# Optimization experiments

Measured on AMD Instinct MI355X. Metric: run time of the kernel, lower is better.

Reference implementation:

```python
import jax, jax.numpy as jnp
import numpy as np


def _approx_match(xyz1, xyz2):
    """Faithful port of approxmatch_cpu/cuda (auction-style soft bipartite matching).

    xyz1: [b, n, 3], xyz2: [b, m, 3] -> (match [b, n, m], sq_dists [b, n, m])
    """
    b, n, _ = xyz1.shape
    m = xyz2.shape[1]
    factorl = max(n, m) // n  # integer division, as in the CUDA source
    factorr = max(n, m) // m

    # all-pairs squared distances  [b, n, m]
    d2 = jnp.sum((xyz1[:, :, None, :] - xyz2[:, None, :, :]) ** 2, axis=-1)

    # annealing schedule: j = 8 .. -1 -> level = -4^j ; j = -2 -> level = 0
    levels = jnp.asarray([-(4.0 ** j) for j in range(8, -2, -1)] + [0.0],
                         dtype=xyz1.dtype)

    satl0 = jnp.full((b, n), float(factorl), dtype=xyz1.dtype)  # row capacities
    satr0 = jnp.full((b, m), float(factorr), dtype=xyz1.dtype)  # col capacities
    match0 = jnp.zeros((b, n, m), dtype=xyz1.dtype)

    def step(carry, level):
        satl, satr, match = carry
        # weight = exp(level * d2) * saturatedr
        w = jnp.exp(level * d2) * satr[:, None, :]                       # [b,n,m]
        # row-normalize, scale by remaining row capacity
        w = w / (jnp.sum(w, axis=2, keepdims=True) + 1e-9) * satl[:, :, None]
        # column rescale by remaining column capacity
        ss = jnp.sum(w, axis=1) + 1e-9                                   # [b,m]
        w = w * (satr / ss)[:, None, :]
        # deplete capacities
        satl = jnp.maximum(satl - jnp.sum(w, axis=2), 0.0)
        satr = jnp.maximum(satr - jnp.sum(w, axis=1), 0.0)
        return (satl, satr, match + w), None

    (_, _, match), _ = jax.lax.scan(step, (satl0, satr0, match0), levels)
    return match, d2


def setup_inputs() -> dict:
    key = jax.random.key(0)
    k1, k2 = jax.random.split(key)
    b, n, m = 4, 4096, 4096
    return {
        "input1": jax.random.normal(k1, (b, n, 3), dtype=jnp.float32),
        "input2": jax.random.normal(k2, (b, m, 3), dtype=jnp.float32),
        "eps": 0,    # accepted but unused by the original Function
        "iters": 50, # accepted but unused by the original Function
    }


def reference(input1, input2, eps, iters):
    # eps / iters are ignored, matching EarthMoverDistanceFunction.apply(xyz1, xyz2)
    match, d2 = _approx_match(input1, input2)
    dist = jnp.sqrt(jnp.maximum(d2, 1e-12))  # matchcost uses euclidean (sqrt) distance
    return jnp.sum(match * dist, axis=(1, 2))  # cost per batch element, [b]
```

## Files before the change

### kernel.cpp

```cpp
#include <hip/hip_runtime.h>

#define BLOCK 256
#define IC    64
#define RPT   4
#define ROWS  (BLOCK*RPT)
#define RBLK  64

__device__ __forceinline__ float wave_reduce_add(float v) {
#pragma unroll
    for (int off = 32; off > 0; off >>= 1) v += __shfl_down(v, off, 64);
    return v;
}
__device__ __forceinline__ float lg2(float x) { return __builtin_amdgcn_logf(x); }
__device__ __forceinline__ float ex2(float x) { return __builtin_amdgcn_exp2f(x); }

__device__ __forceinline__ void load_rows(const float* p, float* x, float* y, float* z) {
    float4 v0 = *(const float4*)p;
    float4 v1 = *(const float4*)(p + 4);
    float4 v2 = *(const float4*)(p + 8);
    x[0]=v0.x; x[1]=v0.w; x[2]=v1.z; x[3]=v2.y;
    y[0]=v0.y; y[1]=v1.x; y[2]=v1.w; y[3]=v2.z;
    z[0]=v0.z; z[1]=v1.y; z[2]=v2.x; z[3]=v2.w;
}

__global__ __launch_bounds__(BLOCK)
void emd_init(float* __restrict__ satl, float* __restrict__ satr,
              float* __restrict__ out, float fl, float fr,
              int b, int n, int m) {
    int idx = blockIdx.x * blockDim.x + threadIdx.x;
    if (idx < b * n) satl[idx] = fl;
    if (idx < b * m) satr[idx] = fr;
    if (idx < b)     out[idx]  = 0.f;
}


__global__ __launch_bounds__(BLOCK, 4)
void emd_pass2(const float* __restrict__ xyzO, const float* __restrict__ xyzS,
               const float* __restrict__ lgw, float* __restrict__ Pout,
               float ls, float wconst, float thr, int nO, int nS, int bnO)
{
    __shared__ float4 sh[IC];
    const int bb = blockIdx.z, chunk = blockIdx.y;

    const int j0 = blockIdx.x * ROWS + threadIdx.x * RPT;
    float x[RPT], y[RPT], z[RPT], acc[RPT];
    load_rows(xyzO + ((size_t)bb * nO + j0) * 3, x, y, z);

    const float* xs = xyzS + (size_t)bb * nS * 3;
    for (int t = threadIdx.x; t < IC; t += BLOCK) {
        int i = chunk * IC + t;
        float w = lgw ? lgw[(size_t)bb * nS + i] : wconst;
        sh[t] = make_float4(xs[3*i], xs[3*i+1], xs[3*i+2], w);
    }
    __syncthreads();

#pragma unroll
    for (int r = 0; r < RPT; ++r) acc[r] = 0.f;
#pragma unroll 2
    for (int tb = 0; tb < IC; tb += 4) {
        float4 q0 = sh[tb+0], q1 = sh[tb+1], q2 = sh[tb+2], q3 = sh[tb+3];
        float d0[RPT], d1[RPT], d2v[RPT], d3[RPT];
        float dmin = 1e30f;
#pragma unroll
        for (int r = 0; r < RPT; ++r) {
            float dx, dy, dz;
            dx=x[r]-q0.x; dy=y[r]-q0.y; dz=z[r]-q0.z; d0[r]=fmaf(dz,dz,fmaf(dy,dy,dx*dx));
            dx=x[r]-q1.x; dy=y[r]-q1.y; dz=z[r]-q1.z; d1[r]=fmaf(dz,dz,fmaf(dy,dy,dx*dx));
            dx=x[r]-q2.x; dy=y[r]-q2.y; dz=z[r]-q2.z; d2v[r]=fmaf(dz,dz,fmaf(dy,dy,dx*dx));
            dx=x[r]-q3.x; dy=y[r]-q3.y; dz=z[r]-q3.z; d3[r]=fmaf(dz,dz,fmaf(dy,dy,dx*dx));
            dmin = fminf(dmin, fminf(fminf(d0[r], d1[r]), fminf(d2v[r], d3[r])));
        }
        if (__any(dmin < thr)) {
#pragma unroll
            for (int r = 0; r < RPT; ++r) {
                acc[r] += ex2(fmaf(d0[r],  ls, q0.w));
                acc[r] += ex2(fmaf(d1[r],  ls, q1.w));
                acc[r] += ex2(fmaf(d2v[r], ls, q2.w));
                acc[r] += ex2(fmaf(d3[r],  ls, q3.w));
            }
        }
    }
    *(float4*)&Pout[(size_t)chunk * bnO + (size_t)bb * nO + j0] =
        make_float4(acc[0], acc[1], acc[2], acc[3]);
}

__global__ __launch_bounds__(BLOCK, 4)
void emd_fused(const float* __restrict__ xyz1, const float* __restrict__ xyz2,
               const float* __restrict__ lgr2, const float* __restrict__ lgsn,
               float* __restrict__ P3a, float* __restrict__ P3b,
               float* __restrict__ P1p,
               float lsA, float lsB, float thr, int n, int m, int bn)
{
    __shared__ float4 sh[IC];
    __shared__ float  shB[IC];
    const int bb = blockIdx.z, chunk = blockIdx.y;

    const int i0 = blockIdx.x * ROWS + threadIdx.x * RPT;
    float x[RPT], y[RPT], z[RPT];
    load_rows(xyz1 + ((size_t)bb * n + i0) * 3, x, y, z);

    const float* x2 = xyz2 + (size_t)bb * m * 3;
    for (int t = threadIdx.x; t < IC; t += BLOCK) {
        int j = chunk * IC + t;
        size_t rj = (size_t)bb * m + j;
        sh[t]  = make_float4(x2[3*j], x2[3*j+1], x2[3*j+2], lgr2[rj]);
        shB[t] = lgsn[rj];
    }
    __syncthreads();

    float s1[RPT], s2[RPT], r1[RPT];
#pragma unroll
    for (int r = 0; r < RPT; ++r) { s1[r] = 0.f; s2[r] = 0.f; r1[r] = 0.f; }
#pragma unroll 2
    for (int tb = 0; tb < IC; tb += 4) {
        float4 q0 = sh[tb+0], q1 = sh[tb+1], q2 = sh[tb+2], q3 = sh[tb+3];
        float lb0 = shB[tb+0], lb1 = shB[tb+1], lb2 = shB[tb+2], lb3 = shB[tb+3];
        float d0[RPT], d1[RPT], d2v[RPT], d3[RPT];
        float dmin = 1e30f;
#pragma unroll
        for (int r = 0; r < RPT; ++r) {
            float dx, dy, dz;
            dx=x[r]-q0.x; dy=y[r]-q0.y; dz=z[r]-q0.z; d0[r]=fmaf(dz,dz,fmaf(dy,dy,dx*dx));
            dx=x[r]-q1.x; dy=y[r]-q1.y; dz=z[r]-q1.z; d1[r]=fmaf(dz,dz,fmaf(dy,dy,dx*dx));
            dx=x[r]-q2.x; dy=y[r]-q2.y; dz=z[r]-q2.z; d2v[r]=fmaf(dz,dz,fmaf(dy,dy,dx*dx));
            dx=x[r]-q3.x; dy=y[r]-q3.y; dz=z[r]-q3.z; d3[r]=fmaf(dz,dz,fmaf(dy,dy,dx*dx));
            dmin = fminf(dmin, fminf(fminf(d0[r], d1[r]), fminf(d2v[r], d3[r])));
        }
        if (__any(dmin < thr)) {
#pragma unroll
            for (int r = 0; r < RPT; ++r) {
                float e;
                e = ex2(fmaf(d0[r], lsA, q0.w));
                s1[r] += e; s2[r] = fmaf(e, __builtin_amdgcn_sqrtf(d0[r]), s2[r]);
                r1[r] += ex2(fmaf(d0[r], lsB, lb0));
                e = ex2(fmaf(d1[r], lsA, q1.w));
                s1[r] += e; s2[r] = fmaf(e, __builtin_amdgcn_sqrtf(d1[r]), s2[r]);
                r1[r] += ex2(fmaf(d1[r], lsB, lb1));
                e = ex2(fmaf(d2v[r], lsA, q2.w));
                s1[r] += e; s2[r] = fmaf(e, __builtin_amdgcn_sqrtf(d2v[r]), s2[r]);
                r1[r] += ex2(fmaf(d2v[r], lsB, lb2));
                e = ex2(fmaf(d3[r], lsA, q3.w));
                s1[r] += e; s2[r] = fmaf(e, __builtin_amdgcn_sqrtf(d3[r]), s2[r]);
                r1[r] += ex2(fmaf(d3[r], lsB, lb3));
            }
        }
    }
    size_t base = (size_t)chunk * bn + (size_t)bb * n + i0;
    *(float4*)&P3a[base] = make_float4(s1[0], s1[1], s1[2], s1[3]);
    *(float4*)&P3b[base] = make_float4(s2[0], s2[1], s2[2], s2[3]);
    *(float4*)&P1p[base] = make_float4(r1[0], r1[1], r1[2], r1[3]);
}

__global__ __launch_bounds__(BLOCK, 4)
void emd_pass3_last(const float* __restrict__ xyz1, const float* __restrict__ xyz2,
                    const float* __restrict__ r2lin, float* __restrict__ P3b,
                    int n, int m, int bn)
{
    __shared__ float4 sh[IC];
    const int bb = blockIdx.z, chunk = blockIdx.y;

    const int i0 = blockIdx.x * ROWS + threadIdx.x * RPT;
    float x[RPT], y[RPT], z[RPT], s2[RPT];
    load_rows(xyz1 + ((size_t)bb * n + i0) * 3, x, y, z);

    const float* x2 = xyz2 + (size_t)bb * m * 3;
    for (int t = threadIdx.x; t < IC; t += BLOCK) {
        int j = chunk * IC + t;
        sh[t] = make_float4(x2[3*j], x2[3*j+1], x2[3*j+2],
                            r2lin[(size_t)bb * m + j]);
    }
    __syncthreads();

#pragma unroll
    for (int r = 0; r < RPT; ++r) s2[r] = 0.f;
#pragma unroll 4
    for (int tb = 0; tb < IC; tb += 4) {
        float4 q0 = sh[tb+0], q1 = sh[tb+1], q2 = sh[tb+2], q3 = sh[tb+3];
#pragma unroll
        for (int r = 0; r < RPT; ++r) {
            float dx, dy, dz, d2;
            dx = x[r]-q0.x; dy = y[r]-q0.y; dz = z[r]-q0.z;
            d2 = fmaf(dz, dz, fmaf(dy, dy, dx*dx));
            s2[r] = fmaf(q0.w, __builtin_amdgcn_sqrtf(d2), s2[r]);
            dx = x[r]-q1.x; dy = y[r]-q1.y; dz = z[r]-q1.z;
            d2 = fmaf(dz, dz, fmaf(dy, dy, dx*dx));
            s2[r] = fmaf(q1.w, __builtin_amdgcn_sqrtf(d2), s2[r]);
            dx = x[r]-q2.x; dy = y[r]-q2.y; dz = z[r]-q2.z;
            d2 = fmaf(dz, dz, fmaf(dy, dy, dx*dx));
            s2[r] = fmaf(q2.w, __builtin_amdgcn_sqrtf(d2), s2[r]);
            dx = x[r]-q3.x; dy = y[r]-q3.y; dz = z[r]-q3.z;
            d2 = fmaf(dz, dz, fmaf(dy, dy, dx*dx));
            s2[r] = fmaf(q3.w, __builtin_amdgcn_sqrtf(d2), s2[r]);
        }
    }
    *(float4*)&P3b[(size_t)chunk * bn + (size_t)bb * n + i0] =
        make_float4(s2[0], s2[1], s2[2], s2[3]);
}


__global__ __launch_bounds__(RBLK)
void emd_redL(float* __restrict__ satl, float* __restrict__ a,
              float* __restrict__ lga,
              const float* __restrict__ P1p, const float* __restrict__ P3a,
              const float* __restrict__ P3b, float* __restrict__ cost,
              int C, int bn, int n, int first)
{
    const int idx = blockIdx.x * RBLK + threadIdx.x;
    float rs = 0.f;
#pragma unroll 16
    for (int c = 0; c < C; ++c) rs += P1p[(size_t)c * bn + idx];
    float sl;
    if (first) {
        sl = satl[idx];
    } else {
        float s1 = 0.f, s2 = 0.f;
#pragma unroll 16
        for (int c = 0; c < C; ++c) {
            s1 += P3a[(size_t)c * bn + idx];
            s2 += P3b[(size_t)c * bn + idx];
        }
        float ap = a[idx];
        sl = fmaxf(satl[idx] - ap * s1, 0.f);
        satl[idx] = sl;
        float cv = wave_reduce_add(ap * s2);
        if (threadIdx.x == 0) atomicAdd(&cost[idx / n], cv);
    }
    float av = sl / (rs + 1e-9f);
    a[idx] = av;
    lga[idx] = lg2(av);
}

__global__ __launch_bounds__(RBLK)
void emd_redR(float* __restrict__ satr, const float* __restrict__ P2p,
              float* __restrict__ lgr2, float* __restrict__ lgsn,
              int C2, int bm, int linear)
{
    const int idx = blockIdx.x * RBLK + threadIdx.x;
    float cs = 0.f;
#pragma unroll 16
    for (int c = 0; c < C2; ++c) cs += P2p[(size_t)c * bm + idx];
    float sr  = satr[idx];
    float cs2 = sr * cs;
    float inv = sr / (cs2 + 1e-9f);
    float r2  = sr * inv;
    float sn  = fmaxf(sr - cs2 * inv, 0.f);
    satr[idx] = sn;
    if (linear) {
        lgr2[idx] = r2;
    } else {
        lgr2[idx] = lg2(r2);
        lgsn[idx] = lg2(sn);
    }
}

__global__ __launch_bounds__(RBLK)
void emd_final(const float* __restrict__ a, const float* __restrict__ P3b,
               float* __restrict__ cost, int C, int bn, int n)
{
    const int idx = blockIdx.x * RBLK + threadIdx.x;
    float s2 = 0.f;
#pragma unroll 16
    for (int c = 0; c < C; ++c) s2 += P3b[(size_t)c * bn + idx];
    float cv = wave_reduce_add(a[idx] * s2);
    if (threadIdx.x == 0) atomicAdd(&cost[idx / n], cv);
}

extern "C" void kernel_launch(void* const* d_in, const int* in_sizes, int n_in,
                              void* d_out, int out_size, void* d_ws, size_t ws_size,
                              hipStream_t stream)
{
    const float* xyz1 = (const float*)d_in[0];
    const float* xyz2 = (const float*)d_in[1];
    const int b = out_size;
    const int n = in_sizes[0] / (3 * b);
    const int m = in_sizes[1] / (3 * b);
    const int C  = m / IC;
    const int C2 = n / IC;
    const int bn = b * n, bm = b * m;

    float* ws   = (float*)d_ws;
    float* satl = ws; ws += (size_t)bn;
    float* satr = ws; ws += (size_t)bm;
    float* aArr = ws; ws += (size_t)bn;
    float* lga  = ws; ws += (size_t)bn;
    float* lgr2 = ws; ws += (size_t)bm;
    float* lgsn = ws; ws += (size_t)bm;
    float* P1p  = ws; ws += (size_t)bn * C;
    float* P2p  = ws; ws += (size_t)bm * C2;
    float* P3a  = ws; ws += (size_t)bn * C;
    float* P3b  = ws; ws += (size_t)bn * C;

    float* out = (float*)d_out;

    const int mx = n > m ? n : m;
    const float fl = (float)(mx / n), fr = (float)(mx / m);
    const float lgfr = log2f(fr);

    emd_init<<<dim3((b * mx + BLOCK - 1) / BLOCK), BLOCK, 0, stream>>>(
        satl, satr, out, fl, fr, b, n, m);

    const double LOG2E = 1.4426950408889634074;
    const double levels[11] = {-65536.0, -16384.0, -4096.0, -1024.0, -256.0,
                               -64.0, -16.0, -4.0, -1.0, -0.25, 0.0};
    float lsv[11], thrP[11], thrF[10];
    for (int k = 0; k < 11; ++k) {
        lsv[k] = (float)(levels[k] * LOG2E);
        thrP[k] = (k <= 4) ? 165.f / fabsf(lsv[k]) : 1e30f;
    }
    for (int k = 0; k < 10; ++k) {
        float tA = 165.f / fabsf(lsv[k]);
        float tB = (k + 1 <= 4) ? 135.f / fabsf(lsv[k + 1]) : 1e30f;
        thrF[k] = (k <= 4) ? fminf(tA, tB) : 1e30f;
    }

    const dim3 g1(n / ROWS, m / IC, b);
    const dim3 g2(m / ROWS, n / IC, b);
    const dim3 gRn(bn / RBLK), gRm(bm / RBLK);

    emd_pass2<<<g1, BLOCK, 0, stream>>>(xyz1, xyz2, (const float*)nullptr, P1p,
                                        lsv[0], lgfr, thrP[0], n, m, bn);
    emd_redL<<<gRn, RBLK, 0, stream>>>(satl, aArr, lga, P1p, P3a, P3b, out,
                                       C, bn, n, 1);
    for (int L = 0; L < 10; ++L) {
        emd_pass2<<<g2, BLOCK, 0, stream>>>(xyz2, xyz1, lga, P2p,
                                            lsv[L], 0.f, thrP[L], m, n, bm);
        emd_redR<<<gRm, RBLK, 0, stream>>>(satr, P2p, lgr2, lgsn, C2, bm, 0);
        emd_fused<<<g1, BLOCK, 0, stream>>>(xyz1, xyz2, lgr2, lgsn,
                                            P3a, P3b, P1p,
                                            lsv[L], lsv[L + 1], thrF[L], n, m, bn);
        emd_redL<<<gRn, RBLK, 0, stream>>>(satl, aArr, lga, P1p, P3a, P3b, out,
                                           C, bn, n, 0);
    }
    emd_pass2<<<g2, BLOCK, 0, stream>>>(xyz2, xyz1, lga, P2p,
                                        lsv[10], 0.f, thrP[10], m, n, bm);
    emd_redR<<<gRm, RBLK, 0, stream>>>(satr, P2p, lgr2, lgsn, C2, bm, 1);
    emd_pass3_last<<<g1, BLOCK, 0, stream>>>(xyz1, xyz2, lgr2, P3b, n, m, bn);
    emd_final<<<gRn, RBLK, 0, stream>>>(aArr, P3b, out, C, bn, n);
}
```

Before: 711.5 us.

## Fuse row/column reduction kernels into the following pairwise passes with ping-pong state

Removes the separate emd_redL/emd_redR reduction kernels. Each pairwise kernel now reduces the partial sums for its own 64-column chunk in shared memory, then updates capacities into double-buffered satl/satr/a arrays (only blockIdx.x==0 writes them). It also adds no-threshold branches for levels where skipping never triggers, lowers the skip cutoff level, and replaces the exp sum at level 0 with a column-capacity sum. This cuts roughly twenty launches and their global round trips, at the cost of every block redundantly re-reducing the partials for its chunk.

```diff
diff --git a/kernel.cpp b/kernel.cpp
--- a/kernel.cpp
+++ b/kernel.cpp
@@ -33,24 +33,22 @@
     if (idx < b)     out[idx]  = 0.f;
 }
 
-
 __global__ __launch_bounds__(BLOCK, 4)
-void emd_pass2(const float* __restrict__ xyzO, const float* __restrict__ xyzS,
-               const float* __restrict__ lgw, float* __restrict__ Pout,
-               float ls, float wconst, float thr, int nO, int nS, int bnO)
+void emd_pass1(const float* __restrict__ xyz1, const float* __restrict__ xyz2,
+               float* __restrict__ P1p, float ls, float wconst, float thr,
+               int n, int m, int bn)
 {
     __shared__ float4 sh[IC];
     const int bb = blockIdx.z, chunk = blockIdx.y;
 
-    const int j0 = blockIdx.x * ROWS + threadIdx.x * RPT;
+    const int i0 = blockIdx.x * ROWS + threadIdx.x * RPT;
     float x[RPT], y[RPT], z[RPT], acc[RPT];
-    load_rows(xyzO + ((size_t)bb * nO + j0) * 3, x, y, z);
-
-    const float* xs = xyzS + (size_t)bb * nS * 3;
+    load_rows(xyz1 + ((size_t)bb * n + i0) * 3, x, y, z);
+
+    const float* x2 = xyz2 + (size_t)bb * m * 3;
     for (int t = threadIdx.x; t < IC; t += BLOCK) {
-        int i = chunk * IC + t;
-        float w = lgw ? lgw[(size_t)bb * nS + i] : wconst;
-        sh[t] = make_float4(xs[3*i], xs[3*i+1], xs[3*i+2], w);
+        int j = chunk * IC + t;
+        sh[t] = make_float4(x2[3*j], x2[3*j+1], x2[3*j+2], wconst);
     }
     __syncthreads();
 
@@ -80,72 +78,270 @@
             }
         }
     }
-    *(float4*)&Pout[(size_t)chunk * bnO + (size_t)bb * nO + j0] =
+    *(float4*)&P1p[(size_t)chunk * bn + (size_t)bb * n + i0] =
+        make_float4(acc[0], acc[1], acc[2], acc[3]);
+}
+
+__global__ __launch_bounds__(BLOCK, 4)
+void emd_pass2(const float* __restrict__ xyzO, const float* __restrict__ xyzS,
+               const float* __restrict__ satlIn, float* __restrict__ satlOut,
+               const float* __restrict__ aIn, float* __restrict__ aOut,
+               const float* __restrict__ P1p, const float* __restrict__ P3a,
+               const float* __restrict__ P3b, float* __restrict__ P2p,
+               float* __restrict__ cost,
+               float ls, float thr, int nO, int nS, int bnS, int bnO,
+               int C4, int first)
+{
+    __shared__ float4 sh[IC];
+    __shared__ float red[3][4][IC];
+    const int bb = blockIdx.z, chunk = blockIdx.y;
+
+    const int j0 = blockIdx.x * ROWS + threadIdx.x * RPT;
+    float x[RPT], y[RPT], z[RPT], acc[RPT];
+    load_rows(xyzO + ((size_t)bb * nO + j0) * 3, x, y, z);
+
+    const int t6 = threadIdx.x & 63, g = threadIdx.x >> 6;
+    const size_t ri = (size_t)bb * nS + chunk * IC + t6;
+    {
+        float ps = 0.f, pa = 0.f, pb = 0.f;
+        const int c0 = g * C4;
+        if (first) {
+#pragma unroll 16
+            for (int k = 0; k < C4; ++k) ps += P1p[(size_t)(c0 + k) * bnS + ri];
+        } else {
+#pragma unroll 16
+            for (int k = 0; k < C4; ++k) {
+                ps += P1p[(size_t)(c0 + k) * bnS + ri];
+                pa += P3a[(size_t)(c0 + k) * bnS + ri];
+                pb += P3b[(size_t)(c0 + k) * bnS + ri];
+            }
+        }
+        red[0][g][t6] = ps; red[1][g][t6] = pa; red[2][g][t6] = pb;
+    }
+    __syncthreads();
+    if (threadIdx.x < IC) {
+        float rs = red[0][0][t6] + red[0][1][t6] + red[0][2][t6] + red[0][3][t6];
+        float sl, costv = 0.f;
+        if (first) {
+            sl = satlIn[ri];
+        } else {
+            float s1 = red[1][0][t6] + red[1][1][t6] + red[1][2][t6] + red[1][3][t6];
+            float s2 = red[2][0][t6] + red[2][1][t6] + red[2][2][t6] + red[2][3][t6];
+            float ap = aIn[ri];
+            sl = fmaxf(satlIn[ri] - ap * s1, 0.f);
+            costv = ap * s2;
+        }
+        float av = sl / (rs + 1e-9f);
+        if (blockIdx.x == 0) {
+            satlOut[ri] = sl;
+            aOut[ri]    = av;
+            if (!first) {
+                float cv = wave_reduce_add(costv);
+                if (t6 == 0) atomicAdd(&cost[bb], cv);
+            }
+        }
+        const float* xs = xyzS + ((size_t)bb * nS + chunk * IC + t6) * 3;
+        sh[t6] = make_float4(xs[0], xs[1], xs[2], lg2(av));
+    }
+    __syncthreads();
+
+#pragma unroll
+    for (int r = 0; r < RPT; ++r) acc[r] = 0.f;
+    if (thr < 1e29f) {
+#pragma unroll 2
+        for (int tb = 0; tb < IC; tb += 4) {
+            float4 q0 = sh[tb+0], q1 = sh[tb+1], q2 = sh[tb+2], q3 = sh[tb+3];
+            float d0[RPT], d1[RPT], d2v[RPT], d3[RPT];
+            float dmin = 1e30f;
+#pragma unroll
+            for (int r = 0; r < RPT; ++r) {
+                float dx, dy, dz;
+                dx=x[r]-q0.x; dy=y[r]-q0.y; dz=z[r]-q0.z; d0[r]=fmaf(dz,dz,fmaf(dy,dy,dx*dx));
+                dx=x[r]-q1.x; dy=y[r]-q1.y; dz=z[r]-q1.z; d1[r]=fmaf(dz,dz,fmaf(dy,dy,dx*dx));
+                dx=x[r]-q2.x; dy=y[r]-q2.y; dz=z[r]-q2.z; d2v[r]=fmaf(dz,dz,fmaf(dy,dy,dx*dx));
+                dx=x[r]-q3.x; dy=y[r]-q3.y; dz=z[r]-q3.z; d3[r]=fmaf(dz,dz,fmaf(dy,dy,dx*dx));
+                dmin = fminf(dmin, fminf(fminf(d0[r], d1[r]), fminf(d2v[r], d3[r])));
+            }
+            if (__any(dmin < thr)) {
+#pragma unroll
+                for (int r = 0; r < RPT; ++r) {
+                    acc[r] += ex2(fmaf(d0[r],  ls, q0.w));
+                    acc[r] += ex2(fmaf(d1[r],  ls, q1.w));
+                    acc[r] += ex2(fmaf(d2v[r], ls, q2.w));
+                    acc[r] += ex2(fmaf(d3[r],  ls, q3.w));
+                }
+            }
+        }
+    } else {
+#pragma unroll 2
+        for (int tb = 0; tb < IC; tb += 4) {
+            float4 q0 = sh[tb+0], q1 = sh[tb+1], q2 = sh[tb+2], q3 = sh[tb+3];
+#pragma unroll
+            for (int r = 0; r < RPT; ++r) {
+                float dx, dy, dz, d2;
+                dx=x[r]-q0.x; dy=y[r]-q0.y; dz=z[r]-q0.z;
+                d2=fmaf(dz,dz,fmaf(dy,dy,dx*dx)); acc[r] += ex2(fmaf(d2, ls, q0.w));
+                dx=x[r]-q1.x; dy=y[r]-q1.y; dz=z[r]-q1.z;
+                d2=fmaf(dz,dz,fmaf(dy,dy,dx*dx)); acc[r] += ex2(fmaf(d2, ls, q1.w));
+                dx=x[r]-q2.x; dy=y[r]-q2.y; dz=z[r]-q2.z;
+                d2=fmaf(dz,dz,fmaf(dy,dy,dx*dx)); acc[r] += ex2(fmaf(d2, ls, q2.w));
+                dx=x[r]-q3.x; dy=y[r]-q3.y; dz=z[r]-q3.z;
+                d2=fmaf(dz,dz,fmaf(dy,dy,dx*dx)); acc[r] += ex2(fmaf(d2, ls, q3.w));
+            }
+        }
+    }
+    *(float4*)&P2p[(size_t)chunk * bnO + (size_t)bb * nO + j0] =
         make_float4(acc[0], acc[1], acc[2], acc[3]);
 }
 
 __global__ __launch_bounds__(BLOCK, 4)
 void emd_fused(const float* __restrict__ xyz1, const float* __restrict__ xyz2,
-               const float* __restrict__ lgr2, const float* __restrict__ lgsn,
+               const float* __restrict__ satrIn, float* __restrict__ satrOut,
+               const float* __restrict__ P2p,
                float* __restrict__ P3a, float* __restrict__ P3b,
                float* __restrict__ P1p,
-               float lsA, float lsB, float thr, int n, int m, int bn)
+               float lsA, float lsB, float thr,
+               int n, int m, int bn, int bm, int C4, int sumOnly)
 {
     __shared__ float4 sh[IC];
     __shared__ float  shB[IC];
+    __shared__ float  red[4][IC];
+    __shared__ float  snsumS;
     const int bb = blockIdx.z, chunk = blockIdx.y;
 
     const int i0 = blockIdx.x * ROWS + threadIdx.x * RPT;
     float x[RPT], y[RPT], z[RPT];
     load_rows(xyz1 + ((size_t)bb * n + i0) * 3, x, y, z);
 
-    const float* x2 = xyz2 + (size_t)bb * m * 3;
-    for (int t = threadIdx.x; t < IC; t += BLOCK) {
-        int j = chunk * IC + t;
-        size_t rj = (size_t)bb * m + j;
-        sh[t]  = make_float4(x2[3*j], x2[3*j+1], x2[3*j+2], lgr2[rj]);
-        shB[t] = lgsn[rj];
+    const int t6 = threadIdx.x & 63, g = threadIdx.x >> 6;
+    const size_t rj = (size_t)bb * m + chunk * IC + t6;
+    {
+        float ps = 0.f;
+        const int c0 = g * C4;
+#pragma unroll 16
+        for (int k = 0; k < C4; ++k) ps += P2p[(size_t)(c0 + k) * bm + rj];
+        red[g][t6] = ps;
+    }
+    __syncthreads();
+    if (threadIdx.x < IC) {
+        float cs  = red[0][t6] + red[1][t6] + red[2][t6] + red[3][t6];
+        float sr  = satrIn[rj];
+        float cs2 = sr * cs;
+        float inv = sr / (cs2 + 1e-9f);
+        float r2  = sr * inv;
+        float sn  = fmaxf(sr - cs2 * inv, 0.f);
+        if (blockIdx.x == 0) satrOut[rj] = sn;
+        const float* xs = xyz2 + ((size_t)bb * m + chunk * IC + t6) * 3;
+        sh[t6]  = make_float4(xs[0], xs[1], xs[2], lg2(r2));
+        shB[t6] = lg2(sn);
+        if (sumOnly) {
+            float ss = wave_reduce_add(sn);
+            if (t6 == 0) snsumS = ss;
+        }
     }
     __syncthreads();
 
     float s1[RPT], s2[RPT], r1[RPT];
 #pragma unroll
     for (int r = 0; r < RPT; ++r) { s1[r] = 0.f; s2[r] = 0.f; r1[r] = 0.f; }
-#pragma unroll 2
-    for (int tb = 0; tb < IC; tb += 4) {
-        float4 q0 = sh[tb+0], q1 = sh[tb+1], q2 = sh[tb+2], q3 = sh[tb+3];
-        float lb0 = shB[tb+0], lb1 = shB[tb+1], lb2 = shB[tb+2], lb3 = shB[tb+3];
-        float d0[RPT], d1[RPT], d2v[RPT], d3[RPT];
-        float dmin = 1e30f;
-#pragma unroll
-        for (int r = 0; r < RPT; ++r) {
-            float dx, dy, dz;
-            dx=x[r]-q0.x; dy=y[r]-q0.y; dz=z[r]-q0.z; d0[r]=fmaf(dz,dz,fmaf(dy,dy,dx*dx));
-            dx=x[r]-q1.x; dy=y[r]-q1.y; dz=z[r]-q1.z; d1[r]=fmaf(dz,dz,fmaf(dy,dy,dx*dx));
-            dx=x[r]-q2.x; dy=y[r]-q2.y; dz=z[r]-q2.z; d2v[r]=fmaf(dz,dz,fmaf(dy,dy,dx*dx));
-            dx=x[r]-q3.x; dy=y[r]-q3.y; dz=z[r]-q3.z; d3[r]=fmaf(dz,dz,fmaf(dy,dy,dx*dx));
-            dmin = fminf(dmin, fminf(fminf(d0[r], d1[r]), fminf(d2v[r], d3[r])));
-        }
-        if (__any(dmin < thr)) {
-#pragma unroll
-            for (int r = 0; r < RPT; ++r) {
-                float e;
-                e = ex2(fmaf(d0[r], lsA, q0.w));
-                s1[r] += e; s2[r] = fmaf(e, __builtin_amdgcn_sqrtf(d0[r]), s2[r]);
-                r1[r] += ex2(fmaf(d0[r], lsB, lb0));
-                e = ex2(fmaf(d1[r], lsA, q1.w));
-                s1[r] += e; s2[r] = fmaf(e, __builtin_amdgcn_sqrtf(d1[r]), s2[r]);
-                r1[r] += ex2(fmaf(d1[r], lsB, lb1));
-                e = ex2(fmaf(d2v[r], lsA, q2.w));
-                s1[r] += e; s2[r] = fmaf(e, __builtin_amdgcn_sqrtf(d2v[r]), s2[r]);
-                r1[r] += ex2(fmaf(d2v[r], lsB, lb2));
-                e = ex2(fmaf(d3[r], lsA, q3.w));
-                s1[r] += e; s2[r] = fmaf(e, __builtin_amdgcn_sqrtf(d3[r]), s2[r]);
-                r1[r] += ex2(fmaf(d3[r], lsB, lb3));
+
+    if (thr < 1e29f) {
+#pragma unroll 2
+        for (int tb = 0; tb < IC; tb += 4) {
+            float4 q0 = sh[tb+0], q1 = sh[tb+1], q2 = sh[tb+2], q3 = sh[tb+3];
+            float lb0 = shB[tb+0], lb1 = shB[tb+1], lb2 = shB[tb+2], lb3 = shB[tb+3];
+            float d0[RPT], d1[RPT], d2v[RPT], d3[RPT];
+            float dmin = 1e30f;
+#pragma unroll
+            for (int r = 0; r < RPT; ++r) {
+                float dx, dy, dz;
+                dx=x[r]-q0.x; dy=y[r]-q0.y; dz=z[r]-q0.z; d0[r]=fmaf(dz,dz,fmaf(dy,dy,dx*dx));
+                dx=x[r]-q1.x; dy=y[r]-q1.y; dz=z[r]-q1.z; d1[r]=fmaf(dz,dz,fmaf(dy,dy,dx*dx));
+                dx=x[r]-q2.x; dy=y[r]-q2.y; dz=z[r]-q2.z; d2v[r]=fmaf(dz,dz,fmaf(dy,dy,dx*dx));
+                dx=x[r]-q3.x; dy=y[r]-q3.y; dz=z[r]-q3.z; d3[r]=fmaf(dz,dz,fmaf(dy,dy,dx*dx));
+                dmin = fminf(dmin, fminf(fminf(d0[r], d1[r]), fminf(d2v[r], d3[r])));
+            }
+            if (__any(dmin < thr)) {
+#pragma unroll
+                for (int r = 0; r < RPT; ++r) {
+                    float e;
+                    e = ex2(fmaf(d0[r], lsA, q0.w));
+                    s1[r] += e; s2[r] = fmaf(e, __builtin_amdgcn_sqrtf(d0[r]), s2[r]);
+                    r1[r] += ex2(fmaf(d0[r], lsB, lb0));
+                    e = ex2(fmaf(d1[r], lsA, q1.w));
+                    s1[r] += e; s2[r] = fmaf(e, __builtin_amdgcn_sqrtf(d1[r]), s2[r]);
+                    r1[r] += ex2(fmaf(d1[r], lsB, lb1));
+                    e = ex2(fmaf(d2v[r], lsA, q2.w));
+                    s1[r] += e; s2[r] = fmaf(e, __builtin_amdgcn_sqrtf(d2v[r]), s2[r]);
+                    r1[r] += ex2(fmaf(d2v[r], lsB, lb2));
+                    e = ex2(fmaf(d3[r], lsA, q3.w));
+                    s1[r] += e; s2[r] = fmaf(e, __builtin_amdgcn_sqrtf(d3[r]), s2[r]);
+                    r1[r] += ex2(fmaf(d3[r], lsB, lb3));
+                }
+            }
+        }
+    } else if (sumOnly) {
+#pragma unroll 2
+        for (int tb = 0; tb < IC; tb += 4) {
+            float4 q0 = sh[tb+0], q1 = sh[tb+1], q2 = sh[tb+2], q3 = sh[tb+3];
+#pragma unroll
+            for (int r = 0; r < RPT; ++r) {
+                float dx, dy, dz, d2, e;
+                dx=x[r]-q0.x; dy=y[r]-q0.y; dz=z[r]-q0.z;
+                d2=fmaf(dz,dz,fmaf(dy,dy,dx*dx));
+                e = ex2(fmaf(d2, lsA, q0.w));
+                s1[r] += e; s2[r] = fmaf(e, __builtin_amdgcn_sqrtf(d2), s2[r]);
+                dx=x[r]-q1.x; dy=y[r]-q1.y; dz=z[r]-q1.z;
+                d2=fmaf(dz,dz,fmaf(dy,dy,dx*dx));
+                e = ex2(fmaf(d2, lsA, q1.w));
+                s1[r] += e; s2[r] = fmaf(e, __builtin_amdgcn_sqrtf(d2), s2[r]);
+                dx=x[r]-q2.x; dy=y[r]-q2.y; dz=z[r]-q2.z;
+                d2=fmaf(dz,dz,fmaf(dy,dy,dx*dx));
+                e = ex2(fmaf(d2, lsA, q2.w));
+                s1[r] += e; s2[r] = fmaf(e, __builtin_amdgcn_sqrtf(d2), s2[r]);
+                dx=x[r]-q3.x; dy=y[r]-q3.y; dz=z[r]-q3.z;
+                d2=fmaf(dz,dz,fmaf(dy,dy,dx*dx));
+                e = ex2(fmaf(d2, lsA, q3.w));
+                s1[r] += e; s2[r] = fmaf(e, __builtin_amdgcn_sqrtf(d2), s2[r]);
+            }
+        }
+    } else {
+#pragma unroll 2
+        for (int tb = 0; tb < IC; tb += 4) {
+            float4 q0 = sh[tb+0], q1 = sh[tb+1], q2 = sh[tb+2], q3 = sh[tb+3];
+            float lb0 = shB[tb+0], lb1 = shB[tb+1], lb2 = shB[tb+2], lb3 = shB[tb+3];
+#pragma unroll
+            for (int r = 0; r < RPT; ++r) {
+                float dx, dy, dz, d2, e;
+                dx=x[r]-q0.x; dy=y[r]-q0.y; dz=z[r]-q0.z;
+                d2=fmaf(dz,dz,fmaf(dy,dy,dx*dx));
+                e = ex2(fmaf(d2, lsA, q0.w));
+                s1[r] += e; s2[r] = fmaf(e, __builtin_amdgcn_sqrtf(d2), s2[r]);
+                r1[r] += ex2(fmaf(d2, lsB, lb0));
+                dx=x[r]-q1.x; dy=y[r]-q1.y; dz=z[r]-q1.z;
+                d2=fmaf(dz,dz,fmaf(dy,dy,dx*dx));
+                e = ex2(fmaf(d2, lsA, q1.w));
+                s1[r] += e; s2[r] = fmaf(e, __builtin_amdgcn_sqrtf(d2), s2[r]);
+                r1[r] += ex2(fmaf(d2, lsB, lb1));
+                dx=x[r]-q2.x; dy=y[r]-q2.y; dz=z[r]-q2.z;
+                d2=fmaf(dz,dz,fmaf(dy,dy,dx*dx));
+                e = ex2(fmaf(d2, lsA, q2.w));
+                s1[r] += e; s2[r] = fmaf(e, __builtin_amdgcn_sqrtf(d2), s2[r]);
+                r1[r] += ex2(fmaf(d2, lsB, lb2));
+                dx=x[r]-q3.x; dy=y[r]-q3.y; dz=z[r]-q3.z;
+                d2=fmaf(dz,dz,fmaf(dy,dy,dx*dx));
+                e = ex2(fmaf(d2, lsA, q3.w));
+                s1[r] += e; s2[r] = fmaf(e, __builtin_amdgcn_sqrtf(d2), s2[r]);
+                r1[r] += ex2(fmaf(d2, lsB, lb3));
             }
         }
     }
     size_t base = (size_t)chunk * bn + (size_t)bb * n + i0;
+    if (sumOnly) {
+        float sc = snsumS;
+#pragma unroll
+        for (int r = 0; r < RPT; ++r) r1[r] = sc;
+    }
     *(float4*)&P3a[base] = make_float4(s1[0], s1[1], s1[2], s1[3]);
     *(float4*)&P3b[base] = make_float4(s2[0], s2[1], s2[2], s2[3]);
     *(float4*)&P1p[base] = make_float4(r1[0], r1[1], r1[2], r1[3]);
@@ -153,21 +349,34 @@
 
 __global__ __launch_bounds__(BLOCK, 4)
 void emd_pass3_last(const float* __restrict__ xyz1, const float* __restrict__ xyz2,
-                    const float* __restrict__ r2lin, float* __restrict__ P3b,
-                    int n, int m, int bn)
+                    const float* __restrict__ satrIn, const float* __restrict__ P2p,
+                    float* __restrict__ P3b, int n, int m, int bn, int bm, int C4)
 {
     __shared__ float4 sh[IC];
+    __shared__ float red[4][IC];
     const int bb = blockIdx.z, chunk = blockIdx.y;
 
     const int i0 = blockIdx.x * ROWS + threadIdx.x * RPT;
     float x[RPT], y[RPT], z[RPT], s2[RPT];
     load_rows(xyz1 + ((size_t)bb * n + i0) * 3, x, y, z);
 
-    const float* x2 = xyz2 + (size_t)bb * m * 3;
-    for (int t = threadIdx.x; t < IC; t += BLOCK) {
-        int j = chunk * IC + t;
-        sh[t] = make_float4(x2[3*j], x2[3*j+1], x2[3*j+2],
-                            r2lin[(size_t)bb * m + j]);
+    const int t6 = threadIdx.x & 63, g = threadIdx.x >> 6;
+    const size_t rj = (size_t)bb * m + chunk * IC + t6;
+    {
+        float ps = 0.f;
+        const int c0 = g * C4;
+#pragma unroll 16
+        for (int k = 0; k < C4; ++k) ps += P2p[(size_t)(c0 + k) * bm + rj];
+        red[g][t6] = ps;
+    }
+    __syncthreads();
+    if (threadIdx.x < IC) {
+        float cs  = red[0][t6] + red[1][t6] + red[2][t6] + red[3][t6];
+        float sr  = satrIn[rj];
+        float cs2 = sr * cs;
+        float inv = sr / (cs2 + 1e-9f);
+        const float* xs = xyz2 + ((size_t)bb * m + chunk * IC + t6) * 3;
+        sh[t6] = make_float4(xs[0], xs[1], xs[2], sr * inv);
     }
     __syncthreads();
 
@@ -197,62 +406,6 @@
         make_float4(s2[0], s2[1], s2[2], s2[3]);
 }
 
-
-__global__ __launch_bounds__(RBLK)
-void emd_redL(float* __restrict__ satl, float* __restrict__ a,
-              float* __restrict__ lga,
-              const float* __restrict__ P1p, const float* __restrict__ P3a,
-              const float* __restrict__ P3b, float* __restrict__ cost,
-              int C, int bn, int n, int first)
-{
-    const int idx = blockIdx.x * RBLK + threadIdx.x;
-    float rs = 0.f;
-#pragma unroll 16
-    for (int c = 0; c < C; ++c) rs += P1p[(size_t)c * bn + idx];
-    float sl;
-    if (first) {
-        sl = satl[idx];
-    } else {
-        float s1 = 0.f, s2 = 0.f;
-#pragma unroll 16
-        for (int c = 0; c < C; ++c) {
-            s1 += P3a[(size_t)c * bn + idx];
-            s2 += P3b[(size_t)c * bn + idx];
-        }
-        float ap = a[idx];
-        sl = fmaxf(satl[idx] - ap * s1, 0.f);
-        satl[idx] = sl;
-        float cv = wave_reduce_add(ap * s2);
-        if (threadIdx.x == 0) atomicAdd(&cost[idx / n], cv);
-    }
-    float av = sl / (rs + 1e-9f);
-    a[idx] = av;
-    lga[idx] = lg2(av);
-}
-
-__global__ __launch_bounds__(RBLK)
-void emd_redR(float* __restrict__ satr, const float* __restrict__ P2p,
-              float* __restrict__ lgr2, float* __restrict__ lgsn,
-              int C2, int bm, int linear)
-{
-    const int idx = blockIdx.x * RBLK + threadIdx.x;
-    float cs = 0.f;
-#pragma unroll 16
-    for (int c = 0; c < C2; ++c) cs += P2p[(size_t)c * bm + idx];
-    float sr  = satr[idx];
-    float cs2 = sr * cs;
-    float inv = sr / (cs2 + 1e-9f);
-    float r2  = sr * inv;
-    float sn  = fmaxf(sr - cs2 * inv, 0.f);
-    satr[idx] = sn;
-    if (linear) {
-        lgr2[idx] = r2;
-    } else {
-        lgr2[idx] = lg2(r2);
-        lgsn[idx] = lg2(sn);
-    }
-}
-
 __global__ __launch_bounds__(RBLK)
 void emd_final(const float* __restrict__ a, const float* __restrict__ P3b,
                float* __restrict__ cost, int C, int bn, int n)
@@ -278,17 +431,17 @@
     const int C2 = n / IC;
     const int bn = b * n, bm = b * m;
 
-    float* ws   = (float*)d_ws;
-    float* satl = ws; ws += (size_t)bn;
-    float* satr = ws; ws += (size_t)bm;
-    float* aArr = ws; ws += (size_t)bn;
-    float* lga  = ws; ws += (size_t)bn;
-    float* lgr2 = ws; ws += (size_t)bm;
-    float* lgsn = ws; ws += (size_t)bm;
-    float* P1p  = ws; ws += (size_t)bn * C;
-    float* P2p  = ws; ws += (size_t)bm * C2;
-    float* P3a  = ws; ws += (size_t)bn * C;
-    float* P3b  = ws; ws += (size_t)bn * C;
+    float* ws    = (float*)d_ws;
+    float* satlA = ws; ws += (size_t)bn;
+    float* satlB = ws; ws += (size_t)bn;
+    float* satrA = ws; ws += (size_t)bm;
+    float* satrB = ws; ws += (size_t)bm;
+    float* aA    = ws; ws += (size_t)bn;
+    float* aB    = ws; ws += (size_t)bn;
+    float* P1p   = ws; ws += (size_t)bn * C;
+    float* P2p   = ws; ws += (size_t)bm * C2;
+    float* P3a   = ws; ws += (size_t)bn * C;
+    float* P3b   = ws; ws += (size_t)bn * C;
 
     float* out = (float*)d_out;
 
@@ -297,7 +450,7 @@
     const float lgfr = log2f(fr);
 
     emd_init<<<dim3((b * mx + BLOCK - 1) / BLOCK), BLOCK, 0, stream>>>(
-        satl, satr, out, fl, fr, b, n, m);
+        satlA, satrA, out, fl, fr, b, n, m);
 
     const double LOG2E = 1.4426950408889634074;
     const double levels[11] = {-65536.0, -16384.0, -4096.0, -1024.0, -256.0,
@@ -305,35 +458,38 @@
     float lsv[11], thrP[11], thrF[10];
     for (int k = 0; k < 11; ++k) {
         lsv[k] = (float)(levels[k] * LOG2E);
-        thrP[k] = (k <= 4) ? 165.f / fabsf(lsv[k]) : 1e30f;
-    }
-    for (int k = 0; k < 10; ++k) {
-        float tA = 165.f / fabsf(lsv[k]);
-        float tB = (k + 1 <= 4) ? 135.f / fabsf(lsv[k + 1]) : 1e30f;
-        thrF[k] = (k <= 4) ? fminf(tA, tB) : 1e30f;
-    }
+        thrP[k] = (k <= 3) ? 165.f / fabsf(lsv[k]) : 1e30f;
+    }
+    for (int k = 0; k < 10; ++k)
+        thrF[k] = (k <= 3) ? 165.f / fabsf(lsv[k]) : 1e30f;
 
     const dim3 g1(n / ROWS, m / IC, b);
     const dim3 g2(m / ROWS, n / IC, b);
-    const dim3 gRn(bn / RBLK), gRm(bm / RBLK);
-
-    emd_pass2<<<g1, BLOCK, 0, stream>>>(xyz1, xyz2, (const float*)nullptr, P1p,
-                                        lsv[0], lgfr, thrP[0], n, m, bn);
-    emd_redL<<<gRn, RBLK, 0, stream>>>(satl, aArr, lga, P1p, P3a, P3b, out,
-                                       C, bn, n, 1);
-    for (int L = 0; L < 10; ++L) {
-        emd_pass2<<<g2, BLOCK, 0, stream>>>(xyz2, xyz1, lga, P2p,
-                                            lsv[L], 0.f, thrP[L], m, n, bm);
-        emd_redR<<<gRm, RBLK, 0, stream>>>(satr, P2p, lgr2, lgsn, C2, bm, 0);
-        emd_fused<<<g1, BLOCK, 0, stream>>>(xyz1, xyz2, lgr2, lgsn,
-                                            P3a, P3b, P1p,
-                                            lsv[L], lsv[L + 1], thrF[L], n, m, bn);
-        emd_redL<<<gRn, RBLK, 0, stream>>>(satl, aArr, lga, P1p, P3a, P3b, out,
-                                           C, bn, n, 0);
-    }
-    emd_pass2<<<g2, BLOCK, 0, stream>>>(xyz2, xyz1, lga, P2p,
-                                        lsv[10], 0.f, thrP[10], m, n, bm);
-    emd_redR<<<gRm, RBLK, 0, stream>>>(satr, P2p, lgr2, lgsn, C2, bm, 1);
-    emd_pass3_last<<<g1, BLOCK, 0, stream>>>(xyz1, xyz2, lgr2, P3b, n, m, bn);
-    emd_final<<<gRn, RBLK, 0, stream>>>(aArr, P3b, out, C, bn, n);
-}
+    const dim3 gRn(bn / RBLK);
+
+    emd_pass1<<<g1, BLOCK, 0, stream>>>(xyz1, xyz2, P1p, lsv[0], lgfr, thrP[0],
+                                        n, m, bn);
+
+    float *slI = satlA, *slO = satlB, *aI = aA, *aO = aB;
+    float *srI = satrA, *srO = satrB;
+    for (int L = 0; L <= 10; ++L) {
+        emd_pass2<<<g2, BLOCK, 0, stream>>>(xyz2, xyz1, slI, slO, aI, aO,
+                                            P1p, P3a, P3b, P2p, out,
+                                            lsv[L], thrP[L], m, n, bn, bm,
+                                            C / 4, (L == 0) ? 1 : 0);
+        { float* t = slI; slI = slO; slO = t; }
+        { float* t = aI;  aI  = aO;  aO  = t; }
+        if (L < 10) {
+            emd_fused<<<g1, BLOCK, 0, stream>>>(xyz1, xyz2, srI, srO, P2p,
+                                                P3a, P3b, P1p,
+                                                lsv[L], lsv[L + 1], thrF[L],
+                                                n, m, bn, bm, C2 / 4,
+                                                (levels[L + 1] == 0.0) ? 1 : 0);
+            { float* t = srI; srI = srO; srO = t; }
+        } else {
+            emd_pass3_last<<<g1, BLOCK, 0, stream>>>(xyz1, xyz2, srI, P2p, P3b,
+                                                     n, m, bn, bm, C2 / 4);
+        }
+    }
+    emd_final<<<gRn, RBLK, 0, stream>>>(aI, P3b, out, C, bn, n);
+}
```

Result: no change. 698.1 us (-1.9%).
